# Kernel tuning notes

Hardware: AMD Instinct MI355X
Metric: run time of the kernel (lower is better)

## Reference

```python
import jax, jax.numpy as jnp
import numpy as np

N_CONS = 10000
N_COLS = 10000
N = N_CONS + N_COLS
E = 200000
NEG_SLOPE = 0.2  # PyG GATConv default negative_slope


def gat_conv(x, edge_index, W, att_src, att_dst, bias, heads, out_ch):
    """PyG-style GATConv (eval mode, add_self_loops=True, concat=True)."""
    n = x.shape[0]
    loops = jnp.arange(n, dtype=edge_index.dtype)
    ei = jnp.concatenate([edge_index, jnp.stack([loops, loops])], axis=1)
    src, dst = ei[0], ei[1]                      # message flows src -> dst
    xp = (x @ W.T).reshape(n, heads, out_ch)     # [N, H, C]
    a_src = jnp.einsum('nhc,hc->nh', xp, att_src)  # [N, H]
    a_dst = jnp.einsum('nhc,hc->nh', xp, att_dst)
    e = jax.nn.leaky_relu(a_src[src] + a_dst[dst], NEG_SLOPE)  # [E', H]
    # segment softmax over edges sharing a destination node
    m = jax.ops.segment_max(e, dst, num_segments=n)
    p = jnp.exp(e - m[dst])
    denom = jax.ops.segment_sum(p, dst, num_segments=n)
    alpha = p / (denom[dst] + 1e-16)
    out = jax.ops.segment_sum(alpha[:, :, None] * xp[src], dst, num_segments=n)
    return out.reshape(n, heads * out_ch) + bias


def setup_inputs() -> dict:
    key = jax.random.key(0)
    ks = jax.random.split(key, 16)
    s = 0.05
    return {
        'constraints_state': jax.random.normal(ks[0], (N_CONS, 4), jnp.float32),
        'columns_state': jax.random.normal(ks[1], (N_COLS, 8), jnp.float32),
        'node_W': jax.random.normal(ks[2], (128, 8), jnp.float32) * s,
        'node_b': jnp.zeros((128,), jnp.float32),
        'col_W': jax.random.normal(ks[3], (128, 16), jnp.float32) * s,
        'col_b': jnp.zeros((128,), jnp.float32),
        'W1': jax.random.normal(ks[4], (1024, 128), jnp.float32) * s,
        'att_src1': jax.random.normal(ks[5], (8, 128), jnp.float32) * s,
        'att_dst1': jax.random.normal(ks[6], (8, 128), jnp.float32) * s,
        'b1': jnp.zeros((1024,), jnp.float32),
        'W2': jax.random.normal(ks[7], (128, 1024), jnp.float32) * s,
        'att_src2': jax.random.normal(ks[8], (1, 128), jnp.float32) * s,
        'att_dst2': jax.random.normal(ks[9], (1, 128), jnp.float32) * s,
        'b2': jnp.zeros((128,), jnp.float32),
        'out_W': jax.random.normal(ks[10], (128, 128), jnp.float32) * s,
        'out_b': jnp.zeros((128,), jnp.float32),
        'edges': jax.random.randint(ks[11], (2, E), 0, N, dtype=jnp.int64),
    }


def reference(constraints_state, columns_state, node_W, node_b, col_W, col_b,
              W1, att_src1, att_dst1, b1, W2, att_src2, att_dst2, b2,
              out_W, out_b, edges):
    # feature_gain=2: repeat features along the feature axis
    nf = jnp.tile(constraints_state, (1, 2))   # [N_CONS, 8]
    cf = jnp.tile(columns_state, (1, 2))       # [N_COLS, 16]
    ne = jax.nn.relu(nf @ node_W.T + node_b)
    ce = jax.nn.relu(cf @ col_W.T + col_b)
    emb = jnp.concatenate([ne, ce], axis=0)    # [N, 128]
    emb = jax.nn.relu(gat_conv(emb, edges, W1, att_src1, att_dst1, b1, 8, 128))
    # torch.flip(edges, [1]) on [2,E] reverses edge ordering (same semantics)
    emb = jax.nn.relu(gat_conv(emb, jnp.flip(edges, axis=1), W2,
                               att_src2, att_dst2, b2, 1, 128))
    logits = emb[-N_COLS:] @ out_W.T + out_b   # [N_COLS, 128]
    return logits
```

## Files before the change

### kernel.cpp

```cpp
#include <hip/hip_runtime.h>

#define NCONS 10000
#define NCOLSN 10000
#define NNODES 20000
#define NEDGE 200000
#define NETOT 220000
#define NEG_SLOPE 0.2f
#define NSCANB 79

typedef unsigned short u16;
typedef __attribute__((ext_vector_type(8))) short bf16x8;
typedef __attribute__((ext_vector_type(4))) float f32x4;

__device__ __forceinline__ float bf2f(u16 u) {
  return __uint_as_float(((unsigned int)u) << 16);
}
__device__ __forceinline__ u16 f2bf(float f) {
  unsigned int x = __float_as_uint(f);
  return (u16)((x + 0x7fffu + ((x >> 16) & 1u)) >> 16);
}
__device__ __forceinline__ float lrelu(float v) {
  return v >= 0.f ? v : NEG_SLOPE * v;
}
__device__ __forceinline__ void gl2lds16(const u16* g, u16* l) {
  __builtin_amdgcn_global_load_lds(
      (const __attribute__((address_space(1))) unsigned int*)g,
      (__attribute__((address_space(3))) unsigned int*)l, 16, 0, 0);
}
__device__ __forceinline__ float readlane_f(float v, int j) {
  return __uint_as_float(__builtin_amdgcn_readlane(__float_as_uint(v), j));
}

#define W1N (1024 * 128)
#define W2N (128 * 1024)
#define OWN (128 * 128)
#define EMB0N (NNODES * 128)
#define WSDN (16 * 128)

__global__ void prep(const float* __restrict__ cons, const float* __restrict__ cols,
                     const float* __restrict__ nW, const float* __restrict__ nb,
                     const float* __restrict__ cW, const float* __restrict__ cb,
                     const float* __restrict__ W1, const float* __restrict__ W2,
                     const float* __restrict__ oW, const float* __restrict__ att_s1,
                     const float* __restrict__ att_d1, u16* __restrict__ emb,
                     u16* __restrict__ Wbf, u16* __restrict__ wsd,
                     const int* __restrict__ edges, int* __restrict__ counts) {
  int idx = blockIdx.x * 256 + threadIdx.x;
  if (idx < NETOT) {
    int dst = (idx < NEDGE) ? edges[NEDGE + idx] : (idx - NEDGE);
    atomicAdd(&counts[dst], 1);
  }
  if (idx < EMB0N) {
    int row = idx >> 7, o = idx & 127;
    float acc;
    if (row < NCONS) {
      acc = nb[o];
      #pragma unroll
      for (int k = 0; k < 4; ++k)
        acc += cons[row * 4 + k] * (nW[o * 8 + k] + nW[o * 8 + 4 + k]);
    } else {
      int r = row - NCONS;
      acc = cb[o];
      #pragma unroll
      for (int k = 0; k < 8; ++k)
        acc += cols[r * 8 + k] * (cW[o * 16 + k] + cW[o * 16 + 8 + k]);
    }
    emb[idx] = f2bf(fmaxf(acc, 0.f));
    return;
  }
  int i = idx - EMB0N;
  if (i < W1N + W2N + OWN) {
    float v;
    if (i < W1N) v = W1[i];
    else if (i < W1N + W2N) v = W2[i - W1N];
    else v = oW[i - W1N - W2N];
    Wbf[i] = f2bf(v);
    return;
  }
  int i2 = i - (W1N + W2N + OWN);
  if (i2 < WSDN) {
    int vec = i2 >> 7, k = i2 & 127;
    int h = vec & 7;
    const float* att = (vec < 8) ? att_s1 : att_d1;
    float a = 0.f;
    #pragma unroll 8
    for (int c = 0; c < 128; ++c)
      a += att[h * 128 + c] * W1[(size_t)(h * 128 + c) * 128 + k];
    wsd[i2] = f2bf(a);
  }
}

__global__ void scan_a(const int* __restrict__ counts, int* __restrict__ lscan,
                       int* __restrict__ bsum) {
  __shared__ int sh[256];
  int t = threadIdx.x;
  int i = blockIdx.x * 256 + t;
  int v = (i < NNODES) ? counts[i] : 0;
  sh[t] = v;
  __syncthreads();
  for (int d = 1; d < 256; d <<= 1) {
    int add = (t >= d) ? sh[t - d] : 0;
    __syncthreads();
    sh[t] += add;
    __syncthreads();
  }
  lscan[i] = sh[t];
  if (t == 255) bsum[blockIdx.x] = sh[255];
}
__global__ void scan_c2(const int* __restrict__ lscan, const int* __restrict__ counts,
                        const int* __restrict__ bsum, int* __restrict__ offsets,
                        int* __restrict__ cursor) {
  __shared__ int sh[128];
  int t = threadIdx.x;
  if (t < 128) sh[t] = (t < NSCANB) ? bsum[t] : 0;
  __syncthreads();
  for (int d = 1; d < 128; d <<= 1) {
    int add = (t >= d && t < 128) ? sh[t - d] : 0;
    __syncthreads();
    if (t < 128) sh[t] += add;
    __syncthreads();
  }
  int bbase = (blockIdx.x > 0) ? sh[blockIdx.x - 1] : 0;
  int i = blockIdx.x * 256 + t;
  if (i == 0) offsets[0] = 0;
  if (i < NNODES) {
    int incl = lscan[i] + bbase;
    offsets[i + 1] = incl;
    cursor[i] = incl - counts[i];
  }
}

__global__ void fill_edges(const int* __restrict__ edges, int* __restrict__ cursor,
                           int* __restrict__ csr_src) {
  int i = blockIdx.x * 256 + threadIdx.x;
  if (i >= NETOT) return;
  int src, dst;
  if (i < NEDGE) { src = edges[i]; dst = edges[NEDGE + i]; }
  else { src = dst = i - NEDGE; }
  int pos = atomicAdd(&cursor[dst], 1);
  csr_src[pos] = src;
}

__global__ __launch_bounds__(256) void dots1_k(const u16* __restrict__ emb,
                                               const u16* __restrict__ wsd,
                                               float* __restrict__ as1,
                                               float* __restrict__ ad1) {
  int wv = threadIdx.x >> 6, lane = threadIdx.x & 63;
  int quad = lane >> 4, l16 = lane & 15;
  int m0 = blockIdx.x * 64 + wv * 16;
  int ra = m0 + l16; if (ra >= NNODES) ra = NNODES - 1;
  f32x4 acc = f32x4{0.f, 0.f, 0.f, 0.f};
  #pragma unroll
  for (int k0 = 0; k0 < 128; k0 += 32) {
    bf16x8 a = *(const bf16x8*)(emb + (size_t)ra * 128 + k0 + quad * 8);
    bf16x8 b = *(const bf16x8*)(wsd + (size_t)l16 * 128 + k0 + quad * 8);
    acc = __builtin_amdgcn_mfma_f32_16x16x32_bf16(a, b, acc, 0, 0, 0);
  }
  #pragma unroll
  for (int r = 0; r < 4; ++r) {
    int node = m0 + quad * 4 + r;
    if (node < NNODES) {
      if (l16 < 8) as1[node * 8 + l16] = acc[r];
      else         ad1[node * 8 + (l16 - 8)] = acc[r];
    }
  }
}

template <int BM, bool SLICED, bool DOTS, bool BIAS, bool RELU, bool OUTF32>
__global__ __launch_bounds__(256) void gemm_bt(const u16* __restrict__ A, const u16* __restrict__ B,
                                               const float* __restrict__ bias, void* __restrict__ Cv,
                                               const float* __restrict__ att_s,
                                               const float* __restrict__ att_d,
                                               float* __restrict__ a_srcO, float* __restrict__ a_dstO,
                                               int M, int N, int K, size_t aSlice) {
  constexpr int MI = BM / 32;
  __shared__ u16 sA[BM * 32];
  __shared__ u16 sB[128 * 32];
  int tid = threadIdx.x;
  int wv = tid >> 6;
  int lane = tid & 63;
  int quad = lane >> 4;
  int l16 = lane & 15;
  int m0 = blockIdx.x * BM;
  int n0g = blockIdx.y * 128;
  int h = n0g >> 7;
  const u16* Ab = SLICED ? A + (size_t)h * aSlice : A;
  const u16* Bb = SLICED ? B + (size_t)h * (size_t)128 * K : B;
  int brow0 = SLICED ? 0 : n0g;
  int rm = (wv >> 1) * (16 * MI);
  int cn = (wv & 1) * 64;

  f32x4 acc[MI][4];
  #pragma unroll
  for (int mi = 0; mi < MI; ++mi)
    #pragma unroll
    for (int ni = 0; ni < 4; ++ni) acc[mi][ni] = f32x4{0.f, 0.f, 0.f, 0.f};

  for (int k0 = 0; k0 < K; k0 += 32) {
    for (int off = tid * 16; off < BM * 64; off += 4096) {
      int row = off >> 6;
      int kk = (off & 63) >> 1;
      int rg = m0 + row; if (rg >= M) rg = M - 1;
      gl2lds16(Ab + (size_t)rg * K + k0 + kk, &sA[off >> 1]);
    }
    for (int off = tid * 16; off < 128 * 64; off += 4096) {
      int row = off >> 6;
      int kk = (off & 63) >> 1;
      gl2lds16(Bb + (size_t)(brow0 + row) * K + k0 + kk, &sB[off >> 1]);
    }
    __syncthreads();
    bf16x8 af[MI], bf[4];
    #pragma unroll
    for (int mi = 0; mi < MI; ++mi)
      af[mi] = *(const bf16x8*)&sA[(rm + mi * 16 + l16) * 32 + quad * 8];
    #pragma unroll
    for (int ni = 0; ni < 4; ++ni)
      bf[ni] = *(const bf16x8*)&sB[(cn + ni * 16 + l16) * 32 + quad * 8];
    #pragma unroll
    for (int mi = 0; mi < MI; ++mi)
      #pragma unroll
      for (int ni = 0; ni < 4; ++ni)
        acc[mi][ni] = __builtin_amdgcn_mfma_f32_16x16x32_bf16(af[mi], bf[ni], acc[mi][ni], 0, 0, 0);
    __syncthreads();
  }

  if (DOTS) {
    float av_s[4], av_d[4];
    #pragma unroll
    for (int ni = 0; ni < 4; ++ni) {
      int col = n0g + cn + ni * 16 + l16;
      av_s[ni] = att_s[col];
      av_d[ni] = att_d[col];
    }
    int H = N >> 7;
    #pragma unroll
    for (int mi = 0; mi < MI; ++mi) {
      #pragma unroll
      for (int r = 0; r < 4; ++r) {
        float sp = 0.f, dp = 0.f;
        #pragma unroll
        for (int ni = 0; ni < 4; ++ni) {
          sp += acc[mi][ni][r] * av_s[ni];
          dp += acc[mi][ni][r] * av_d[ni];
        }
        #pragma unroll
        for (int w = 1; w < 16; w <<= 1) {
          sp += __shfl_xor(sp, w, 64);
          dp += __shfl_xor(dp, w, 64);
        }
        int orow = m0 + rm + mi * 16 + quad * 4 + r;
        if (l16 == 0 && orow < M) {
          atomicAdd(&a_srcO[(size_t)orow * H + h], sp);
          atomicAdd(&a_dstO[(size_t)orow * H + h], dp);
        }
      }
    }
  }
  #pragma unroll
  for (int ni = 0; ni < 4; ++ni) {
    int col = n0g + cn + ni * 16 + l16;
    float bv = BIAS ? bias[col] : 0.f;
    #pragma unroll
    for (int mi = 0; mi < MI; ++mi) {
      #pragma unroll
      for (int r = 0; r < 4; ++r) {
        int orow = m0 + rm + mi * 16 + quad * 4 + r;
        if (orow < M) {
          float v = acc[mi][ni][r] + bv;
          if (RELU) v = fmaxf(v, 0.f);
          if (OUTF32) ((float*)Cv)[(size_t)orow * N + col] = v;
          else        ((u16*)Cv)[(size_t)orow * N + col] = f2bf(v);
        }
      }
    }
  }
}

__global__ __launch_bounds__(256) void alpha1_k(const int* __restrict__ offs,
                                                const int* __restrict__ csr_src,
                                                const float* __restrict__ a_src,
                                                const float* __restrict__ a_dst,
                                                float* __restrict__ alpha) {
  int wv = threadIdx.x >> 6;
  int dst = blockIdx.x * 4 + wv;
  if (dst >= NNODES) return;
  int l = threadIdx.x & 63;
  int h = l & 7, i = l >> 3;
  int off = offs[dst];
  int deg = offs[dst + 1] - off;
  const int* srcs = csr_src + off;
  float ad = a_dst[dst * 8 + h];
  float m = -1e30f, ssum = 0.f;
  float* out = alpha + (size_t)off * 8;
  if (deg <= 64) {
    int sl = srcs[l < deg ? l : deg - 1];
    float g[8];
    #pragma unroll
    for (int t = 0; t < 8; ++t) {
      int jj = i + t * 8;
      int s = __builtin_amdgcn_readlane(sl, jj < deg ? jj : 0);
      g[t] = a_src[s * 8 + h];
    }
    float ev[8];
    #pragma unroll
    for (int t = 0; t < 8; ++t) {
      int jj = i + t * 8;
      float e = (jj < deg) ? lrelu(g[t] + ad) : -1e30f;
      ev[t] = e;
      float nm = fmaxf(m, e);
      ssum = ssum * __expf(m - nm) + ((jj < deg) ? __expf(e - nm) : 0.f);
      m = nm;
    }
    #pragma unroll
    for (int w = 8; w < 64; w <<= 1) {
      float om = __shfl_xor(m, w, 64);
      float os = __shfl_xor(ssum, w, 64);
      float nm = fmaxf(m, om);
      ssum = ssum * __expf(m - nm) + os * __expf(om - nm);
      m = nm;
    }
    float inv = 1.f / (ssum + 1e-16f);
    #pragma unroll
    for (int t = 0; t < 8; ++t) {
      int jj = i + t * 8;
      if (jj < deg) out[(size_t)jj * 8 + h] = __expf(ev[t] - m) * inv;
    }
  } else {
    for (int j = i; j < deg; j += 8) {
      int s = srcs[j];
      float e = lrelu(a_src[s * 8 + h] + ad);
      float nm = fmaxf(m, e);
      ssum = ssum * __expf(m - nm) + __expf(e - nm);
      m = nm;
    }
    #pragma unroll
    for (int w = 8; w < 64; w <<= 1) {
      float om = __shfl_xor(m, w, 64);
      float os = __shfl_xor(ssum, w, 64);
      float nm = fmaxf(m, om);
      ssum = ssum * __expf(m - nm) + os * __expf(om - nm);
      m = nm;
    }
    float inv = 1.f / (ssum + 1e-16f);
    for (int j = i; j < deg; j += 8) {
      int s = srcs[j];
      float e = lrelu(a_src[s * 8 + h] + ad);
      out[(size_t)j * 8 + h] = __expf(e - m) * inv;
    }
  }
}

__global__ __launch_bounds__(256) void magg1(const int* __restrict__ offs,
                                             const int* __restrict__ csr_src,
                                             const float* __restrict__ alp,
                                             const u16* __restrict__ emb,
                                             u16* __restrict__ aggh) {
  int wvi = threadIdx.x >> 6;
  int dst = blockIdx.x * 4 + wvi;
  if (dst >= NNODES) return;
  int l = threadIdx.x & 63;
  int off = offs[dst];
  int deg = offs[dst + 1] - off;
  const int* srcs = csr_src + off;
  const u16* base = emb + l * 2;
  float acc[8][2];
  #pragma unroll
  for (int h = 0; h < 8; ++h) { acc[h][0] = 0.f; acc[h][1] = 0.f; }
  for (int b0 = 0; b0 < deg; b0 += 64) {
    int cnt = deg - b0; if (cnt > 64) cnt = 64;
    int sv = srcs[b0 + (l < cnt ? l : cnt - 1)];
    int g0 = 0;
    for (; g0 + 8 <= cnt; g0 += 8) {
      float av = alp[(size_t)(off + b0 + g0) * 8 + l];
      ushort2 uu[8];
      #pragma unroll
      for (int t = 0; t < 8; ++t) {
        int s = __builtin_amdgcn_readlane(sv, g0 + t);
        uu[t] = *(const ushort2*)(base + (size_t)s * 128);
      }
      #pragma unroll
      for (int t = 0; t < 8; ++t) {
        float x0 = bf2f(uu[t].x), x1 = bf2f(uu[t].y);
        #pragma unroll
        for (int h = 0; h < 8; ++h) {
          float w = readlane_f(av, t * 8 + h);
          acc[h][0] += w * x0;
          acc[h][1] += w * x1;
        }
      }
    }
    if (g0 < cnt) {
      int ei = g0 + (l >> 3);
      float av = (ei < cnt) ? alp[(size_t)(off + b0 + ei) * 8 + (l & 7)] : 0.f;
      int gn = cnt - g0;
      ushort2 uu[8];
      for (int t = 0; t < gn; ++t) {
        int s = __builtin_amdgcn_readlane(sv, g0 + t);
        uu[t] = *(const ushort2*)(base + (size_t)s * 128);
      }
      for (int t = 0; t < gn; ++t) {
        float x0 = bf2f(uu[t].x), x1 = bf2f(uu[t].y);
        #pragma unroll
        for (int h = 0; h < 8; ++h) {
          float w = readlane_f(av, t * 8 + h);
          acc[h][0] += w * x0;
          acc[h][1] += w * x1;
        }
      }
    }
  }
  #pragma unroll
  for (int h = 0; h < 8; ++h) {
    ushort2 o;
    o.x = f2bf(acc[h][0]);
    o.y = f2bf(acc[h][1]);
    *(ushort2*)(aggh + (size_t)h * ((size_t)NNODES * 128) + (size_t)dst * 128 + l * 2) = o;
  }
}

__global__ __launch_bounds__(256) void fsp2(const int* __restrict__ offs,
                                            const int* __restrict__ csr_src,
                                            const float* __restrict__ a_src,
                                            const float* __restrict__ a_dst,
                                            const u16* __restrict__ xp2,
                                            const float* __restrict__ bias,
                                            u16* __restrict__ out) {
  int wvi = threadIdx.x >> 6;
  int dst = NCONS + blockIdx.x * 4 + wvi;
  if (dst >= NNODES) return;
  int l = threadIdx.x & 63;
  int off = offs[dst];
  int deg = offs[dst + 1] - off;
  const int* srcs = csr_src + off;
  float ad = a_dst[dst];
  const u16* base = xp2 + l * 2;
  float m = -1e30f, ssum = 0.f, a0 = 0.f, a1 = 0.f;
  for (int b0 = 0; b0 < deg; b0 += 64) {
    int cnt = deg - b0; if (cnt > 64) cnt = 64;
    int sv = srcs[b0 + (l < cnt ? l : cnt - 1)];
    float e = (l < cnt) ? lrelu(a_src[sv] + ad) : -1e30f;
    float mc = e;
    #pragma unroll
    for (int w = 1; w < 64; w <<= 1) mc = fmaxf(mc, __shfl_xor(mc, w, 64));
    float pex = __expf(e - mc);
    float sc = pex;
    #pragma unroll
    for (int w = 1; w < 64; w <<= 1) sc += __shfl_xor(sc, w, 64);
    float c0 = 0.f, c1 = 0.f;
    int j = 0;
    for (; j + 8 <= cnt; j += 8) {
      ushort2 uu[8];
      float ww[8];
      #pragma unroll
      for (int t = 0; t < 8; ++t) {
        int s = __builtin_amdgcn_readlane(sv, j + t);
        ww[t] = readlane_f(pex, j + t);
        uu[t] = *(const ushort2*)(base + (size_t)s * 128);
      }
      #pragma unroll
      for (int t = 0; t < 8; ++t) {
        c0 += ww[t] * bf2f(uu[t].x);
        c1 += ww[t] * bf2f(uu[t].y);
      }
    }
    for (; j < cnt; ++j) {
      int s = __builtin_amdgcn_readlane(sv, j);
      float w = readlane_f(pex, j);
      ushort2 u = *(const ushort2*)(base + (size_t)s * 128);
      c0 += w * bf2f(u.x);
      c1 += w * bf2f(u.y);
    }
    float nm = fmaxf(m, mc);
    float fo = __expf(m - nm), fn = __expf(mc - nm);
    a0 = a0 * fo + c0 * fn;
    a1 = a1 * fo + c1 * fn;
    ssum = ssum * fo + sc * fn;
    m = nm;
  }
  float inv = 1.f / (ssum + 1e-16f);
  int cg = l * 2;
  ushort2 o;
  o.x = f2bf(fmaxf(a0 * inv + bias[cg], 0.f));
  o.y = f2bf(fmaxf(a1 * inv + bias[cg + 1], 0.f));
  *(ushort2*)(out + (size_t)dst * 128 + cg) = o;
}

extern "C" void kernel_launch(void* const* d_in, const int* in_sizes, int n_in,
                              void* d_out, int out_size, void* d_ws, size_t ws_size,
                              hipStream_t stream) {
  const float* cons    = (const float*)d_in[0];
  const float* cols    = (const float*)d_in[1];
  const float* node_W  = (const float*)d_in[2];
  const float* node_b  = (const float*)d_in[3];
  const float* col_W   = (const float*)d_in[4];
  const float* col_b   = (const float*)d_in[5];
  const float* W1      = (const float*)d_in[6];
  const float* att_s1  = (const float*)d_in[7];
  const float* att_d1  = (const float*)d_in[8];
  const float* b1      = (const float*)d_in[9];
  const float* W2      = (const float*)d_in[10];
  const float* att_s2  = (const float*)d_in[11];
  const float* att_d2  = (const float*)d_in[12];
  const float* b2      = (const float*)d_in[13];
  const float* out_W   = (const float*)d_in[14];
  const float* out_b   = (const float*)d_in[15];
  const int* edges     = (const int*)d_in[16];

  char* p = (char*)d_ws;
  auto alloc = [&](size_t bytes) {
    char* r = p;
    p += (bytes + 255) & ~(size_t)255;
    return r;
  };
  u16* emb0    = (u16*)alloc((size_t)NNODES * 128 * 2);
  u16* aggh    = (u16*)alloc((size_t)8 * NNODES * 128 * 2);
  u16* emb2    = (u16*)alloc((size_t)NNODES * 1024 * 2);
  u16* xp2     = (u16*)alloc((size_t)NNODES * 128 * 2);
  u16* emb3    = (u16*)alloc((size_t)NNODES * 128 * 2);
  u16* Wbf     = (u16*)alloc((size_t)(W1N + W2N + OWN) * 2);
  u16* wsd     = (u16*)alloc((size_t)WSDN * 2);
  float* as2   = (float*)alloc((size_t)NNODES * 4);
  float* ad2   = (float*)alloc((size_t)NNODES * 4);
  int* counts  = (int*)alloc((size_t)NNODES * 4);
  size_t zspan = (char*)(counts + NNODES) - (char*)as2;
  float* as1   = (float*)alloc((size_t)NNODES * 8 * 4);
  float* ad1   = (float*)alloc((size_t)NNODES * 8 * 4);
  float* alp1  = (float*)alloc((size_t)NETOT * 8 * 4);
  int* offs    = (int*)alloc((size_t)(NNODES + 1) * 4);
  int* cursor  = (int*)alloc((size_t)NNODES * 4);
  int* csrsrc  = (int*)alloc((size_t)NETOT * 4);
  int* lscan   = (int*)alloc((size_t)NSCANB * 256 * 4);
  int* bsum    = (int*)alloc((size_t)NSCANB * 4);

  u16* W1bf = Wbf;
  u16* W2bf = Wbf + W1N;
  u16* oWbf = Wbf + W1N + W2N;

  hipMemsetAsync(as2, 0, zspan, stream);

  prep<<<(EMB0N + W1N + W2N + OWN + WSDN + 255) / 256, 256, 0, stream>>>(
      cons, cols, node_W, node_b, col_W, col_b, W1, W2, out_W, att_s1, att_d1,
      emb0, Wbf, wsd, edges, counts);

  scan_a<<<NSCANB, 256, 0, stream>>>(counts, lscan, bsum);
  scan_c2<<<NSCANB, 256, 0, stream>>>(lscan, counts, bsum, offs, cursor);
  fill_edges<<<(NETOT + 255) / 256, 256, 0, stream>>>(edges, cursor, csrsrc);

  dots1_k<<<(NNODES + 63) / 64, 256, 0, stream>>>(emb0, wsd, as1, ad1);
  alpha1_k<<<(NNODES + 3) / 4, 256, 0, stream>>>(offs, csrsrc, as1, ad1, alp1);
  magg1<<<(NNODES + 3) / 4, 256, 0, stream>>>(offs, csrsrc, alp1, emb0, aggh);
  gemm_bt<128, true, false, true, true, false><<<dim3((NNODES + 127) / 128, 8), 256, 0, stream>>>(
      aggh, W1bf, b1, emb2, nullptr, nullptr, nullptr, nullptr,
      NNODES, 1024, 128, (size_t)NNODES * 128);

  gemm_bt<32, false, true, false, false, false><<<dim3((NNODES + 31) / 32, 1), 256, 0, stream>>>(
      emb2, W2bf, nullptr, xp2, att_s2, att_d2, as2, ad2, NNODES, 128, 1024, 0);
  fsp2<<<(NCOLSN + 3) / 4, 256, 0, stream>>>(offs, csrsrc, as2, ad2, xp2, b2, emb3);

  gemm_bt<32, false, false, true, false, true><<<dim3((NCOLSN + 31) / 32, 1), 256, 0, stream>>>(
      emb3 + (size_t)NCONS * 128, oWbf, out_b, d_out, nullptr, nullptr, nullptr, nullptr,
      NCOLSN, 128, 128, 0);
}
```

Baseline: 261.9 us.

## Fuse layer-1 attention softmax into aggregation kernel via LDS weights

Merges the alpha computation kernel and the message aggregation kernel into one per-destination kernel. The normalized attention weights now stay in per-wave shared memory instead of a global alpha buffer of edges×8 floats, which removes one launch and the global write and read of that buffer. The aggregation output is also stored node-major as [N,1024] instead of per-head slices. The GEMM gains an lda/offset parameter so it can read each head's slice from that layout. The risks are extra LDS reads inside the inner accumulation loop and a strided A access in the first GEMM.

```diff
diff --git a/kernel.cpp b/kernel.cpp
--- a/kernel.cpp
+++ b/kernel.cpp
@@ -172,7 +172,7 @@
                                                const float* __restrict__ att_s,
                                                const float* __restrict__ att_d,
                                                float* __restrict__ a_srcO, float* __restrict__ a_dstO,
-                                               int M, int N, int K, size_t aSlice) {
+                                               int M, int N, int K, int lda, size_t aOff) {
   constexpr int MI = BM / 32;
   __shared__ u16 sA[BM * 32];
   __shared__ u16 sB[128 * 32];
@@ -184,7 +184,7 @@
   int m0 = blockIdx.x * BM;
   int n0g = blockIdx.y * 128;
   int h = n0g >> 7;
-  const u16* Ab = SLICED ? A + (size_t)h * aSlice : A;
+  const u16* Ab = SLICED ? A + (size_t)h * aOff : A;
   const u16* Bb = SLICED ? B + (size_t)h * (size_t)128 * K : B;
   int brow0 = SLICED ? 0 : n0g;
   int rm = (wv >> 1) * (16 * MI);
@@ -201,7 +201,7 @@
       int row = off >> 6;
       int kk = (off & 63) >> 1;
       int rg = m0 + row; if (rg >= M) rg = M - 1;
-      gl2lds16(Ab + (size_t)rg * K + k0 + kk, &sA[off >> 1]);
+      gl2lds16(Ab + (size_t)rg * lda + k0 + kk, &sA[off >> 1]);
     }
     for (int off = tid * 16; off < 128 * 64; off += 4096) {
       int row = off >> 6;
@@ -276,36 +276,42 @@
   }
 }
 
-__global__ __launch_bounds__(256) void alpha1_k(const int* __restrict__ offs,
-                                                const int* __restrict__ csr_src,
-                                                const float* __restrict__ a_src,
-                                                const float* __restrict__ a_dst,
-                                                float* __restrict__ alpha) {
-  int wv = threadIdx.x >> 6;
-  int dst = blockIdx.x * 4 + wv;
+__global__ __launch_bounds__(256) void fagg1(const int* __restrict__ offs,
+                                             const int* __restrict__ csr_src,
+                                             const float* __restrict__ as1,
+                                             const float* __restrict__ ad1,
+                                             const u16* __restrict__ emb,
+                                             u16* __restrict__ agg) {
+  __shared__ float alds[4 * 512];
+  int wvi = threadIdx.x >> 6;
+  int dst = blockIdx.x * 4 + wvi;
   if (dst >= NNODES) return;
   int l = threadIdx.x & 63;
   int h = l & 7, i = l >> 3;
+  float* wlds = &alds[wvi * 512];
   int off = offs[dst];
   int deg = offs[dst + 1] - off;
   const int* srcs = csr_src + off;
-  float ad = a_dst[dst * 8 + h];
-  float m = -1e30f, ssum = 0.f;
-  float* out = alpha + (size_t)off * 8;
+  float adv = ad1[dst * 8 + h];
+  const u16* base = emb + l * 2;
+  float acc[8][2];
+  #pragma unroll
+  for (int hh = 0; hh < 8; ++hh) { acc[hh][0] = 0.f; acc[hh][1] = 0.f; }
+
   if (deg <= 64) {
     int sl = srcs[l < deg ? l : deg - 1];
     float g[8];
     #pragma unroll
     for (int t = 0; t < 8; ++t) {
-      int jj = i + t * 8;
+      int jj = t * 8 + i;
       int s = __builtin_amdgcn_readlane(sl, jj < deg ? jj : 0);
-      g[t] = a_src[s * 8 + h];
-    }
-    float ev[8];
+      g[t] = as1[s * 8 + h];
+    }
+    float m = -1e30f, ssum = 0.f, ev[8];
     #pragma unroll
     for (int t = 0; t < 8; ++t) {
-      int jj = i + t * 8;
-      float e = (jj < deg) ? lrelu(g[t] + ad) : -1e30f;
+      int jj = t * 8 + i;
+      float e = (jj < deg) ? lrelu(g[t] + adv) : -1e30f;
       ev[t] = e;
       float nm = fmaxf(m, e);
       ssum = ssum * __expf(m - nm) + ((jj < deg) ? __expf(e - nm) : 0.f);
@@ -321,14 +327,33 @@
     }
     float inv = 1.f / (ssum + 1e-16f);
     #pragma unroll
-    for (int t = 0; t < 8; ++t) {
-      int jj = i + t * 8;
-      if (jj < deg) out[(size_t)jj * 8 + h] = __expf(ev[t] - m) * inv;
+    for (int t = 0; t < 8; ++t)
+      wlds[t * 64 + l] = __expf(ev[t] - m) * inv;
+    for (int j0 = 0; j0 < deg; j0 += 8) {
+      ushort2 uu[8];
+      #pragma unroll
+      for (int t2 = 0; t2 < 8; ++t2) {
+        int slot = j0 + t2;
+        int s = __builtin_amdgcn_readlane(sl, slot < deg ? slot : 0);
+        uu[t2] = *(const ushort2*)(base + (size_t)s * 128);
+      }
+      #pragma unroll
+      for (int t2 = 0; t2 < 8; ++t2) {
+        int slot = j0 + t2;
+        float x0 = bf2f(uu[t2].x), x1 = bf2f(uu[t2].y);
+        #pragma unroll
+        for (int hh = 0; hh < 8; ++hh) {
+          float w = wlds[slot * 8 + hh];
+          acc[hh][0] += w * x0;
+          acc[hh][1] += w * x1;
+        }
+      }
     }
   } else {
+    float m = -1e30f, ssum = 0.f;
     for (int j = i; j < deg; j += 8) {
       int s = srcs[j];
-      float e = lrelu(a_src[s * 8 + h] + ad);
+      float e = lrelu(as1[s * 8 + h] + adv);
       float nm = fmaxf(m, e);
       ssum = ssum * __expf(m - nm) + __expf(e - nm);
       m = nm;
@@ -342,79 +367,47 @@
       m = nm;
     }
     float inv = 1.f / (ssum + 1e-16f);
-    for (int j = i; j < deg; j += 8) {
-      int s = srcs[j];
-      float e = lrelu(a_src[s * 8 + h] + ad);
-      out[(size_t)j * 8 + h] = __expf(e - m) * inv;
-    }
-  }
-}
-
-__global__ __launch_bounds__(256) void magg1(const int* __restrict__ offs,
-                                             const int* __restrict__ csr_src,
-                                             const float* __restrict__ alp,
-                                             const u16* __restrict__ emb,
-                                             u16* __restrict__ aggh) {
-  int wvi = threadIdx.x >> 6;
-  int dst = blockIdx.x * 4 + wvi;
-  if (dst >= NNODES) return;
-  int l = threadIdx.x & 63;
-  int off = offs[dst];
-  int deg = offs[dst + 1] - off;
-  const int* srcs = csr_src + off;
-  const u16* base = emb + l * 2;
-  float acc[8][2];
+    for (int b0 = 0; b0 < deg; b0 += 64) {
+      int cnt = deg - b0; if (cnt > 64) cnt = 64;
+      #pragma unroll
+      for (int t = 0; t < 8; ++t) {
+        int sl2 = t * 8 + i;
+        float a = 0.f;
+        if (sl2 < cnt) {
+          int s = srcs[b0 + sl2];
+          a = __expf(lrelu(as1[s * 8 + h] + adv) - m) * inv;
+        }
+        wlds[t * 64 + l] = a;
+      }
+      int sv = srcs[b0 + (l < cnt ? l : cnt - 1)];
+      for (int j0 = 0; j0 < cnt; j0 += 8) {
+        ushort2 uu[8];
+        #pragma unroll
+        for (int t2 = 0; t2 < 8; ++t2) {
+          int slot = j0 + t2;
+          int s = __builtin_amdgcn_readlane(sv, slot < cnt ? slot : 0);
+          uu[t2] = *(const ushort2*)(base + (size_t)s * 128);
+        }
+        #pragma unroll
+        for (int t2 = 0; t2 < 8; ++t2) {
+          int slot = j0 + t2;
+          float x0 = bf2f(uu[t2].x), x1 = bf2f(uu[t2].y);
+          #pragma unroll
+          for (int hh = 0; hh < 8; ++hh) {
+            float w = wlds[slot * 8 + hh];
+            acc[hh][0] += w * x0;
+            acc[hh][1] += w * x1;
+          }
+        }
+      }
+    }
+  }
   #pragma unroll
-  for (int h = 0; h < 8; ++h) { acc[h][0] = 0.f; acc[h][1] = 0.f; }
-  for (int b0 = 0; b0 < deg; b0 += 64) {
-    int cnt = deg - b0; if (cnt > 64) cnt = 64;
-    int sv = srcs[b0 + (l < cnt ? l : cnt - 1)];
-    int g0 = 0;
-    for (; g0 + 8 <= cnt; g0 += 8) {
-      float av = alp[(size_t)(off + b0 + g0) * 8 + l];
-      ushort2 uu[8];
-      #pragma unroll
-      for (int t = 0; t < 8; ++t) {
-        int s = __builtin_amdgcn_readlane(sv, g0 + t);
-        uu[t] = *(const ushort2*)(base + (size_t)s * 128);
-      }
-      #pragma unroll
-      for (int t = 0; t < 8; ++t) {
-        float x0 = bf2f(uu[t].x), x1 = bf2f(uu[t].y);
-        #pragma unroll
-        for (int h = 0; h < 8; ++h) {
-          float w = readlane_f(av, t * 8 + h);
-          acc[h][0] += w * x0;
-          acc[h][1] += w * x1;
-        }
-      }
-    }
-    if (g0 < cnt) {
-      int ei = g0 + (l >> 3);
-      float av = (ei < cnt) ? alp[(size_t)(off + b0 + ei) * 8 + (l & 7)] : 0.f;
-      int gn = cnt - g0;
-      ushort2 uu[8];
-      for (int t = 0; t < gn; ++t) {
-        int s = __builtin_amdgcn_readlane(sv, g0 + t);
-        uu[t] = *(const ushort2*)(base + (size_t)s * 128);
-      }
-      for (int t = 0; t < gn; ++t) {
-        float x0 = bf2f(uu[t].x), x1 = bf2f(uu[t].y);
-        #pragma unroll
-        for (int h = 0; h < 8; ++h) {
-          float w = readlane_f(av, t * 8 + h);
-          acc[h][0] += w * x0;
-          acc[h][1] += w * x1;
-        }
-      }
-    }
-  }
-  #pragma unroll
-  for (int h = 0; h < 8; ++h) {
+  for (int hh = 0; hh < 8; ++hh) {
     ushort2 o;
-    o.x = f2bf(acc[h][0]);
-    o.y = f2bf(acc[h][1]);
-    *(ushort2*)(aggh + (size_t)h * ((size_t)NNODES * 128) + (size_t)dst * 128 + l * 2) = o;
+    o.x = f2bf(acc[hh][0]);
+    o.y = f2bf(acc[hh][1]);
+    *(ushort2*)(agg + (size_t)dst * 1024 + hh * 128 + l * 2) = o;
   }
 }
 
@@ -513,7 +506,7 @@
     return r;
   };
   u16* emb0    = (u16*)alloc((size_t)NNODES * 128 * 2);
-  u16* aggh    = (u16*)alloc((size_t)8 * NNODES * 128 * 2);
+  u16* agg     = (u16*)alloc((size_t)NNODES * 1024 * 2);
   u16* emb2    = (u16*)alloc((size_t)NNODES * 1024 * 2);
   u16* xp2     = (u16*)alloc((size_t)NNODES * 128 * 2);
   u16* emb3    = (u16*)alloc((size_t)NNODES * 128 * 2);
@@ -525,7 +518,6 @@
   size_t zspan = (char*)(counts + NNODES) - (char*)as2;
   float* as1   = (float*)alloc((size_t)NNODES * 8 * 4);
   float* ad1   = (float*)alloc((size_t)NNODES * 8 * 4);
-  float* alp1  = (float*)alloc((size_t)NETOT * 8 * 4);
   int* offs    = (int*)alloc((size_t)(NNODES + 1) * 4);
   int* cursor  = (int*)alloc((size_t)NNODES * 4);
   int* csrsrc  = (int*)alloc((size_t)NETOT * 4);
@@ -547,17 +539,16 @@
   fill_edges<<<(NETOT + 255) / 256, 256, 0, stream>>>(edges, cursor, csrsrc);
 
   dots1_k<<<(NNODES + 63) / 64, 256, 0, stream>>>(emb0, wsd, as1, ad1);
-  alpha1_k<<<(NNODES + 3) / 4, 256, 0, stream>>>(offs, csrsrc, as1, ad1, alp1);
-  magg1<<<(NNODES + 3) / 4, 256, 0, stream>>>(offs, csrsrc, alp1, emb0, aggh);
+  fagg1<<<(NNODES + 3) / 4, 256, 0, stream>>>(offs, csrsrc, as1, ad1, emb0, agg);
   gemm_bt<128, true, false, true, true, false><<<dim3((NNODES + 127) / 128, 8), 256, 0, stream>>>(
-      aggh, W1bf, b1, emb2, nullptr, nullptr, nullptr, nullptr,
-      NNODES, 1024, 128, (size_t)NNODES * 128);
+      agg, W1bf, b1, emb2, nullptr, nullptr, nullptr, nullptr,
+      NNODES, 1024, 128, 1024, 128);
 
   gemm_bt<32, false, true, false, false, false><<<dim3((NNODES + 31) / 32, 1), 256, 0, stream>>>(
-      emb2, W2bf, nullptr, xp2, att_s2, att_d2, as2, ad2, NNODES, 128, 1024, 0);
+      emb2, W2bf, nullptr, xp2, att_s2, att_d2, as2, ad2, NNODES, 128, 1024, 1024, 0);
   fsp2<<<(NCOLSN + 3) / 4, 256, 0, stream>>>(offs, csrsrc, as2, ad2, xp2, b2, emb3);
 
   gemm_bt<32, false, false, true, false, true><<<dim3((NCOLSN + 31) / 32, 1), 256, 0, stream>>>(
       emb3 + (size_t)NCONS * 128, oWbf, out_b, d_out, nullptr, nullptr, nullptr, nullptr,
-      NCOLSN, 128, 128, 0);
-}
+      NCOLSN, 128, 128, 128, 0);
+}
```

New measurement: 244.2 us. 1.07x faster.
